# Optimization experiments

Measured on AMD Instinct MI355X. Metric: run time of the kernel, lower is better.

Reference implementation:

```python
import jax, jax.numpy as jnp
from jax import lax
import numpy as np

RADIUS = 1
DILATION = 2
NUM_BINS = 16  # DualSimilarityLoss uses num_bins=16
ALPHA = 5.0
BETA = 0.1
NOISE = 1e-4


def _avg_pool2(x):
    b, c, h, w = x.shape
    return x.reshape(b, c, h // 2, 2, w // 2, 2).mean(axis=(3, 5))


def _conv_rep(x, k, pad):
    # replicate-pad then VALID conv, NCHW / OIHW
    xp = jnp.pad(x, ((0, 0), (0, 0), (pad, pad), (pad, pad)), mode='edge')
    return lax.conv_general_dilated(xp, k, (1, 1), 'VALID',
                                    dimension_numbers=('NCHW', 'OIHW', 'NCHW'))


def _upsample_align_corners(x, H, W):
    # bilinear, align_corners=True (matches F.interpolate(..., align_corners=True))
    b, c, h, w = x.shape

    def coords(n_out, n_in):
        pos = jnp.arange(n_out, dtype=x.dtype) * ((n_in - 1) / (n_out - 1))
        i0 = jnp.clip(jnp.floor(pos).astype(jnp.int32), 0, n_in - 2)
        return i0, pos - i0.astype(x.dtype)

    y0, fy = coords(H, h)
    x0, fx = coords(W, w)
    rows = x[:, :, y0, :] * (1.0 - fy)[None, None, :, None] \
         + x[:, :, y0 + 1, :] * fy[None, None, :, None]
    out = rows[:, :, :, x0] * (1.0 - fx) + rows[:, :, :, x0 + 1] * fx
    return out


def _compute_mind(img, key):
    B, _, H, W = img.shape
    img = _avg_pool2(img)                      # (B,1,H/2,W/2)
    img = img + NOISE * jax.random.normal(key, img.shape, img.dtype)
    h, w = img.shape[2], img.shape[3]
    pad = RADIUS * DILATION                    # 2
    k = 2 * RADIUS + 1                         # 3
    ones_k = jnp.ones((1, 1, k, k), img.dtype)
    padded = jnp.pad(img, ((0, 0), (0, 0), (pad, pad), (pad, pad)), mode='edge')
    patch_mean = lax.conv_general_dilated(padded, ones_k, (1, 1), 'VALID',
                                          dimension_numbers=('NCHW', 'OIHW', 'NCHW')) / (k * k)
    patch_mean = jnp.pad(patch_mean, ((0, 0), (0, 0), (pad, pad), (pad, pad)), mode='edge')
    c = pad
    center = padded[:, :, c:c + h, c:c + w]
    variance = (center - patch_mean[:, :, c:c + h, c:c + w]) ** 2
    variance = _conv_rep(variance, ones_k, RADIUS) / (k * k)
    variance = jnp.maximum(variance, 1e-4)
    descs = []
    for i in range(-RADIUS, RADIUS + 1):
        for j in range(-RADIUS, RADIUS + 1):
            if i == 0 and j == 0:
                continue
            dx, dy = i * DILATION, j * DILATION
            off = padded[:, :, c + dy:c + dy + h, c + dx:c + dx + w]
            diff = jnp.clip((center - off) ** 2 / (variance * 2 + 1e-6), 0.0, 50.0)
            descs.append(diff)
    m = jnp.exp(-jnp.concatenate(descs, axis=1))          # (B,8,h,w)
    m = m / (m.sum(axis=1, keepdims=True) + 1e-8)
    m = jnp.where(jnp.isnan(m), 0.0, m)
    if (h, w) != (H, W):
        m = _upsample_align_corners(m, H, W)
    return m


def _nmi_loss(x, y, kx, ky):
    B = x.shape[0]
    x = x[:, :, ::2, ::2]
    y = y[:, :, ::2, ::2]
    x = x + NOISE * jax.random.normal(kx, x.shape, x.dtype)
    y = y + NOISE * jax.random.normal(ky, y.shape, y.dtype)
    xf = jnp.clip((x.reshape(B, -1) + 1.0) / 2.0, 0.001, 0.999)
    yf = jnp.clip((y.reshape(B, -1) + 1.0) / 2.0, 0.001, 0.999)
    grid = jnp.linspace(0.0, 1.0, NUM_BINS + 1)
    xb = jnp.clip(jnp.searchsorted(grid, xf, side='left') - 1, 0, NUM_BINS - 1)
    yb = jnp.clip(jnp.searchsorted(grid, yf, side='left') - 1, 0, NUM_BINS - 1)
    idx = xb * NUM_BINS + yb                               # (B,N)
    hist = jnp.zeros((B, NUM_BINS * NUM_BINS), jnp.float32)
    hist = hist.at[jnp.arange(B)[:, None], idx].add(1.0)
    hist = hist.reshape(B, NUM_BINS, NUM_BINS)
    hist = hist / (hist.sum(axis=(1, 2), keepdims=True) + 1e-10)
    xh = hist.sum(axis=2)
    yh = hist.sum(axis=1)
    eps = 1e-5
    hist = hist + eps
    xh = xh + eps
    yh = yh + eps
    mi = jnp.sum(hist * (jnp.log(hist) - jnp.log(xh[:, :, None] * yh[:, None, :])), axis=(1, 2))
    hx = -jnp.sum(xh * jnp.log(xh), axis=1)
    hy = -jnp.sum(yh * jnp.log(yh), axis=1)
    se = hx + hy
    nmi = jnp.where(se < 1e-10, 0.0, 2.0 * mi / se)
    nmi = jnp.clip(nmi, -1.0, 1.0)
    return -jnp.clip(nmi.mean(), -1.0, 1.0)


def _reg_loss(flow, ku, kv):
    sx = jnp.array([[-1, 0, 1], [-2, 0, 2], [-1, 0, 1]], jnp.float32).reshape(1, 1, 3, 3)
    sy = jnp.array([[-1, -2, -1], [0, 0, 0], [1, 2, 1]], jnp.float32).reshape(1, 1, 3, 3)
    lp = jnp.array([[0, 1, 0], [1, -4, 1], [0, 1, 0]], jnp.float32).reshape(1, 1, 3, 3)
    f = _avg_pool2(flow)
    u = f[:, 0:1] + NOISE * jax.random.normal(ku, f[:, 0:1].shape, f.dtype)
    v = f[:, 1:2] + NOISE * jax.random.normal(kv, f[:, 1:2].shape, f.dtype)
    grad_mag = _conv_rep(u, sx, 1) ** 2 + _conv_rep(u, sy, 1) ** 2 \
             + _conv_rep(v, sx, 1) ** 2 + _conv_rep(v, sy, 1) ** 2
    lap_mag = _conv_rep(u, lp, 1) ** 2 + _conv_rep(v, lp, 1) ** 2
    return jnp.clip(grad_mag, 0.0, 100.0).mean() + jnp.clip(lap_mag, 0.0, 100.0).mean()


def _total_loss(fixed, moved, flow):
    fixed = jnp.where(jnp.isnan(fixed), 0.0, fixed)
    moved = jnp.where(jnp.isnan(moved), 0.0, moved)
    flow = jnp.where(jnp.isnan(flow), 0.0, flow)
    ks = jax.random.split(jax.random.key(42), 6)
    mi = _nmi_loss(fixed, moved, ks[0], ks[1])
    mx = _compute_mind(fixed, ks[2])
    my = _compute_mind(moved, ks[3])
    d = jnp.abs(mx - my)
    mind = jnp.where(jnp.isnan(d), 0.0, d).mean()
    reg = _reg_loss(flow, ks[4], ks[5])
    return mi + ALPHA * mind + BETA * reg


def setup_inputs() -> dict:
    key = jax.random.key(0)
    k1, k2, k3 = jax.random.split(key, 3)
    B, H, W = 8, 512, 512
    return {
        'fixed': jax.random.normal(k1, (B, 1, H, W), jnp.float32),
        'moved': jax.random.normal(k2, (B, 1, H, W), jnp.float32),
        'flow': jax.random.normal(k3, (B, 2, H, W), jnp.float32),
    }


def reference(fixed, moved, flow):
    return _total_loss(fixed, moved, flow)
```

## Files before the change

### kernel.cpp

```cpp
#include <hip/hip_runtime.h>
#include <cmath>

#define BATCH 8
#define HF 512
#define WF 512
#define HS 256
#define WS 256
#define PLANE_S (HS * WS)
#define PLANE_F (HF * WF)

#define NMIND_BLOCKS 2048
#define NREG_BLOCKS  512

#define OFF_HISTP 0
#define OFF_PMIND (2048 * 1024)
#define OFF_PGRAD (OFF_PMIND + NMIND_BLOCKS * 8)
#define OFF_PLAP  (OFF_PGRAD + NREG_BLOCKS * 8)
#define OFF_NMI   (OFF_PLAP + NREG_BLOCKS * 8)

#define IMG_R 23
#define IMG_S 24
#define T_R 20
#define T_S 21
#define V_R 18
#define V_S 19

#define RP 34
#define RS 35

__device__ __forceinline__ int clampi(int v, int lo, int hi) {
    return v < lo ? lo : (v > hi ? hi : v);
}

__device__ __forceinline__ int bin_of(float x) {
    float v = (x + 1.0f) * 0.5f;
    v = fminf(fmaxf(v, 0.001f), 0.999f);
    float t = v * 16.0f;
    float ft = floorf(t);
    int c = (int)ft + ((t > ft) ? 1 : 0);
    int b = c - 1;
    return b < 0 ? 0 : (b > 15 ? 15 : b);
}

__global__ __launch_bounds__(256, 4) void fused_main_kernel(
    const float* __restrict__ fixed, const float* __restrict__ moved,
    const float* __restrict__ flow,
    unsigned* __restrict__ hist_part, double* __restrict__ pmind,
    double* __restrict__ pgrad, double* __restrict__ plap)
{
    __shared__ float S[4524];
    __shared__ unsigned lh[256];
    __shared__ float red[256];
    int tid = threadIdx.x;

    if (blockIdx.z < 2) {
        int idx = blockIdx.z * 256 + blockIdx.y * 16 + blockIdx.x;
        int b = idx >> 6, t64 = idx & 63;
        int y0p = (t64 >> 3) * 32, x0p = (t64 & 7) * 32;
        float* U = S;
        float* V = S + RP * RS;
        const float* ur = flow + (size_t)(b * 2) * PLANE_F;
        const float* vr = ur + PLANE_F;
        for (int i = tid; i < RP * RP; i += 256) {
            int r = i / RP, c = i - r * RP;
            int gy = clampi(y0p - 1 + r, 0, HS - 1);
            int gx = clampi(x0p - 1 + c, 0, WS - 1);
            const float* uu = ur + (size_t)(gy * 2) * WF + (size_t)(gx * 2);
            const float* vv = vr + (size_t)(gy * 2) * WF + (size_t)(gx * 2);
            float2 u0 = *(const float2*)uu, u1 = *(const float2*)(uu + WF);
            float2 v0 = *(const float2*)vv, v1 = *(const float2*)(vv + WF);
            U[r * RS + c] = (u0.x + u0.y + u1.x + u1.y) * 0.25f;
            V[r * RS + c] = (v0.x + v0.y + v1.x + v1.y) * 0.25f;
        }
        __syncthreads();
        float g = 0.f, l = 0.f;
        for (int k = tid; k < 32 * 32; k += 256) {
            int y = k >> 5, x = k & 31;
            const float* u0 = &U[y * RS + x];
            const float* v0 = &V[y * RS + x];
            float a00 = u0[0],      a01 = u0[1],          a02 = u0[2];
            float a10 = u0[RS],     a11 = u0[RS + 1],     a12 = u0[RS + 2];
            float a20 = u0[2 * RS], a21 = u0[2 * RS + 1], a22 = u0[2 * RS + 2];
            float c00 = v0[0],      c01 = v0[1],          c02 = v0[2];
            float c10 = v0[RS],     c11 = v0[RS + 1],     c12 = v0[RS + 2];
            float c20 = v0[2 * RS], c21 = v0[2 * RS + 1], c22 = v0[2 * RS + 2];
            float gxu = (a02 - a00) + 2.f * (a12 - a10) + (a22 - a20);
            float gyu = (a20 - a00) + 2.f * (a21 - a01) + (a22 - a02);
            float gxv = (c02 - c00) + 2.f * (c12 - c10) + (c22 - c20);
            float gyv = (c20 - c00) + 2.f * (c21 - c01) + (c22 - c02);
            float lpu = a01 + a10 - 4.f * a11 + a12 + a21;
            float lpv = c01 + c10 - 4.f * c11 + c12 + c21;
            float grad = gxu * gxu + gyu * gyu + gxv * gxv + gyv * gyv;
            float lap = lpu * lpu + lpv * lpv;
            g += fminf(grad, 100.f);
            l += fminf(lap, 100.f);
        }
        red[tid] = g;
        __syncthreads();
        for (int s = 128; s > 0; s >>= 1) { if (tid < s) red[tid] += red[tid + s]; __syncthreads(); }
        if (tid == 0) pgrad[b * 64 + t64] = (double)red[0];
        __syncthreads();
        red[tid] = l;
        __syncthreads();
        for (int s = 128; s > 0; s >>= 1) { if (tid < s) red[tid] += red[tid + s]; __syncthreads(); }
        if (tid == 0) plap[b * 64 + t64] = (double)red[0];
        return;
    }

    const float FS = (float)(255.0 / 511.0);
    int tx = blockIdx.x, ty = blockIdx.y, b = blockIdx.z - 2;
    int Xb = tx * 32, Yb = ty * 32;
    int dbx = (int)((float)Xb * FS);
    int dby = (int)((float)Yb * FS);
    int ibx = dbx - 3, iby = dby - 3;

    float* imgF = S;
    float* imgM = S + IMG_R * IMG_S;
    float* varF = S + 2 * IMG_R * IMG_S;
    float* varM = varF + V_R * V_S;
    float* diff = varM + V_R * V_S;
    float* tF   = diff;
    float* tM   = diff + T_R * T_S;

    lh[tid] = 0u;
    __syncthreads();

    const float* fb = fixed + (size_t)b * PLANE_F;
    const float* mb = moved + (size_t)b * PLANE_F;
    int oy0 = ty * 16, ox0 = tx * 16;
    for (int i = tid; i < IMG_R * IMG_R; i += 256) {
        int r = i / IMG_R, c = i - r * IMG_R;
        int gy = iby + r, gx = ibx + c;
        int cy = clampi(gy, 0, HS - 1), cx = clampi(gx, 0, WS - 1);
        const float* fp = fb + (size_t)(cy * 2) * WF + (size_t)(cx * 2);
        const float* mp = mb + (size_t)(cy * 2) * WF + (size_t)(cx * 2);
        float2 f0 = *(const float2*)fp;
        float2 f1 = *(const float2*)(fp + WF);
        float2 m0 = *(const float2*)mp;
        float2 m1 = *(const float2*)(mp + WF);
        imgF[r * IMG_S + c] = (f0.x + f0.y + f1.x + f1.y) * 0.25f;
        imgM[r * IMG_S + c] = (m0.x + m0.y + m1.x + m1.y) * 0.25f;
        if ((unsigned)(gy - oy0) < 16u && (unsigned)(gx - ox0) < 16u) {
            atomicAdd(&lh[bin_of(f0.x) * 16 + bin_of(m0.x)], 1u);
        }
    }
    __syncthreads();
    hist_part[((size_t)(b * 256 + ty * 16 + tx)) * 256 + tid] = lh[tid];

    const float NINTH = 1.0f / 9.0f;
    for (int i = tid; i < T_R * T_R; i += 256) {
        int r = i / T_R, c = i - r * T_R;
        float sF = 0.f, sM = 0.f;
        #pragma unroll
        for (int dy = 0; dy < 3; dy++)
            #pragma unroll
            for (int dx = 0; dx < 3; dx++) {
                sF += imgF[(r + dy) * IMG_S + c + dx];
                sM += imgM[(r + dy) * IMG_S + c + dx];
            }
        float dF = imgF[(r + 2) * IMG_S + c + 2] - sF * NINTH;
        float dM = imgM[(r + 2) * IMG_S + c + 2] - sM * NINTH;
        tF[r * T_S + c] = dF * dF;
        tM[r * T_S + c] = dM * dM;
    }
    __syncthreads();

    for (int i = tid; i < V_R * V_R; i += 256) {
        int r = i / V_R, c = i - r * V_R;
        float sF = 0.f, sM = 0.f;
        #pragma unroll
        for (int dy = 0; dy < 3; dy++)
            #pragma unroll
            for (int dx = 0; dx < 3; dx++) {
                sF += tF[(r + dy) * T_S + c + dx];
                sM += tM[(r + dy) * T_S + c + dx];
            }
        varF[r * V_S + c] = fmaxf(sF * NINTH, 1e-4f);
        varM[r * V_S + c] = fmaxf(sM * NINTH, 1e-4f);
    }
    __syncthreads();

    for (int i = tid; i < V_R * V_R; i += 256) {
        int r = i / V_R, c = i - r * V_R;
        float cF = imgF[(r + 3) * IMG_S + c + 3];
        float cM = imgM[(r + 3) * IMG_S + c + 3];
        float dF2 = 2.f * varF[r * V_S + c] + 1e-6f;
        float dM2 = 2.f * varM[r * V_S + c] + 1e-6f;
        float invF = 1.0f / dF2;
        float invM = 1.0f / dM2;
        float eF[8], eM[8];
        float sF = 0.f, sM = 0.f;
        int ch = 0;
        #pragma unroll
        for (int ii = -1; ii <= 1; ii++) {
            #pragma unroll
            for (int jj = -1; jj <= 1; jj++) {
                if (ii == 0 && jj == 0) continue;
                float aF = cF - imgF[(r + 3 + 2 * jj) * IMG_S + (c + 3 + 2 * ii)];
                float aM = cM - imgM[(r + 3 + 2 * jj) * IMG_S + (c + 3 + 2 * ii)];
                float qF = fminf(aF * aF * invF, 50.f);
                float qM = fminf(aM * aM * invM, 50.f);
                float vF_ = expf(-qF), vM_ = expf(-qM);
                eF[ch] = vF_; eM[ch] = vM_;
                sF += vF_; sM += vM_;
                ch++;
            }
        }
        float wF = 1.f / (sF + 1e-8f);
        float wM = 1.f / (sM + 1e-8f);
        float* dp = diff + (size_t)(r * V_S + c) * 8;
        #pragma unroll
        for (int q = 0; q < 8; q++) dp[q] = eF[q] * wF - eM[q] * wM;
    }
    __syncthreads();

    float local = 0.f;
    for (int k = tid; k < 32 * 32; k += 256) {
        int dy = k >> 5, dx = k & 31;
        float py = (float)(Yb + dy) * FS;
        int y0 = (int)py; if (y0 > HS - 2) y0 = HS - 2;
        float fy = py - (float)y0;
        float px = (float)(Xb + dx) * FS;
        int x0 = (int)px; if (x0 > WS - 2) x0 = WS - 2;
        float fx = px - (float)x0;
        const float* p00 = diff + (size_t)((y0 - dby) * V_S + (x0 - dbx)) * 8;
        const float* p10 = p00 + V_S * 8;
        #pragma unroll
        for (int q = 0; q < 8; q++) {
            float a  = p00[q]     * (1.f - fy) + p10[q]     * fy;
            float c2 = p00[q + 8] * (1.f - fy) + p10[q + 8] * fy;
            local += fabsf(a * (1.f - fx) + c2 * fx);
        }
    }
    red[tid] = local;
    __syncthreads();
    for (int s = 128; s > 0; s >>= 1) { if (tid < s) red[tid] += red[tid + s]; __syncthreads(); }
    if (tid == 0) pmind[b * 256 + ty * 16 + tx] = (double)red[0];
}

__global__ void nmi_kernel(const unsigned* __restrict__ hist_part, float* __restrict__ nmi_out) {
    int b = blockIdx.x;
    int t = threadIdx.x;
    __shared__ float p[256];
    __shared__ float xh[16], yh[16];
    __shared__ float red[256];
    unsigned hv = 0;
    const unsigned* hp = hist_part + (size_t)b * 256 * 256 + t;
    for (int i = 0; i < 256; i++) hv += hp[i * 256];
    float pv = (float)hv / 65536.0f;
    p[t] = pv;
    __syncthreads();
    if (t < 16) {
        float s = 0.f;
        for (int j = 0; j < 16; j++) s += p[t * 16 + j];
        xh[t] = s;
    } else if (t < 32) {
        int j = t - 16;
        float s = 0.f;
        for (int i = 0; i < 16; i++) s += p[i * 16 + j];
        yh[j] = s;
    }
    __syncthreads();
    const float eps = 1e-5f;
    int i = t >> 4, j = t & 15;
    float h = pv + eps;
    float mi_term = h * (logf(h) - logf((xh[i] + eps) * (yh[j] + eps)));
    red[t] = mi_term;
    __syncthreads();
    for (int s = 128; s > 0; s >>= 1) { if (t < s) red[t] += red[t + s]; __syncthreads(); }
    float mi = red[0];
    __syncthreads();
    float e_term = 0.f;
    if (t < 16) { float xe = xh[t] + eps; e_term = -xe * logf(xe); }
    else if (t < 32) { float ye = yh[t - 16] + eps; e_term = -ye * logf(ye); }
    red[t] = e_term;
    __syncthreads();
    for (int s = 128; s > 0; s >>= 1) { if (t < s) red[t] += red[t + s]; __syncthreads(); }
    if (t == 0) {
        float se = red[0];
        float nmi = (se < 1e-10f) ? 0.f : 2.f * mi / se;
        nmi_out[b] = fminf(fmaxf(nmi, -1.f), 1.f);
    }
}

__global__ void final_kernel(const float* __restrict__ nmi, const double* __restrict__ pmind,
                             const double* __restrict__ pgrad, const double* __restrict__ plap,
                             float* __restrict__ out) {
    __shared__ double red[256];
    int t = threadIdx.x;
    double sm = 0.0;
    for (int i = t; i < NMIND_BLOCKS; i += 256) sm += pmind[i];
    double sg = 0.0, sl = 0.0;
    for (int i = t; i < NREG_BLOCKS; i += 256) { sg += pgrad[i]; sl += plap[i]; }
    red[t] = sm;
    __syncthreads();
    for (int s = 128; s > 0; s >>= 1) { if (t < s) red[t] += red[t + s]; __syncthreads(); }
    double mind_sum = red[0];
    __syncthreads();
    red[t] = sg;
    __syncthreads();
    for (int s = 128; s > 0; s >>= 1) { if (t < s) red[t] += red[t + s]; __syncthreads(); }
    double grad_sum = red[0];
    __syncthreads();
    red[t] = sl;
    __syncthreads();
    for (int s = 128; s > 0; s >>= 1) { if (t < s) red[t] += red[t + s]; __syncthreads(); }
    double lap_sum = red[0];
    if (t == 0) {
        float s = 0.f;
        for (int b = 0; b < BATCH; b++) s += nmi[b];
        s /= (float)BATCH;
        s = fminf(fmaxf(s, -1.f), 1.f);
        double mi_loss = -(double)s;
        double mind_mean = mind_sum / (64.0 * (double)PLANE_F);
        double reg = grad_sum / (double)(BATCH * PLANE_S) + lap_sum / (double)(BATCH * PLANE_S);
        out[0] = (float)(mi_loss + 5.0 * mind_mean + 0.1 * reg);
    }
}

extern "C" void kernel_launch(void* const* d_in, const int* in_sizes, int n_in,
                              void* d_out, int out_size, void* d_ws, size_t ws_size,
                              hipStream_t stream) {
    const float* fixed = (const float*)d_in[0];
    const float* moved = (const float*)d_in[1];
    const float* flow  = (const float*)d_in[2];
    float* out = (float*)d_out;
    char* ws = (char*)d_ws;

    unsigned* hist_part = (unsigned*)(ws + OFF_HISTP);
    double*   pmind     = (double*)(ws + OFF_PMIND);
    double*   pgrad     = (double*)(ws + OFF_PGRAD);
    double*   plap      = (double*)(ws + OFF_PLAP);
    float*    nmi       = (float*)(ws + OFF_NMI);

    fused_main_kernel<<<dim3(16, 16, 10), 256, 0, stream>>>(fixed, moved, flow,
                                                            hist_part, pmind, pgrad, plap);
    nmi_kernel<<<BATCH, 256, 0, stream>>>(hist_part, nmi);
    final_kernel<<<1, 256, 0, stream>>>(nmi, pmind, pgrad, plap, out);
}
```

Baseline: 112.5 us.

## Accumulate joint histogram with global atomics and merge NMI into final kernel

Each block now adds its local histogram into a per-batch global histogram with atomics instead of writing a 2 MB partial histogram array. This removes the per-batch reduction over 256 partials. The separate NMI and final kernels are merged into one single-block tail kernel, and a small zero-init kernel is added. The cost is atomic contention on 8x256 counters and an extra tiny launch, in exchange for less global traffic and one fewer reduction kernel.

Result: slower. 121.7 us (+8.2%).

```diff
diff --git a/kernel.cpp b/kernel.cpp
--- a/kernel.cpp
+++ b/kernel.cpp
@@ -12,11 +12,10 @@
 #define NMIND_BLOCKS 2048
 #define NREG_BLOCKS  512
 
-#define OFF_HISTP 0
-#define OFF_PMIND (2048 * 1024)
+#define OFF_HIST  0
+#define OFF_PMIND 8192
 #define OFF_PGRAD (OFF_PMIND + NMIND_BLOCKS * 8)
 #define OFF_PLAP  (OFF_PGRAD + NREG_BLOCKS * 8)
-#define OFF_NMI   (OFF_PLAP + NREG_BLOCKS * 8)
 
 #define IMG_R 23
 #define IMG_S 24
@@ -42,10 +41,14 @@
     return b < 0 ? 0 : (b > 15 ? 15 : b);
 }
 
+__global__ void init_hist_kernel(unsigned* __restrict__ hist) {
+    hist[blockIdx.x * 256 + threadIdx.x] = 0u;
+}
+
 __global__ __launch_bounds__(256, 4) void fused_main_kernel(
     const float* __restrict__ fixed, const float* __restrict__ moved,
     const float* __restrict__ flow,
-    unsigned* __restrict__ hist_part, double* __restrict__ pmind,
+    unsigned* __restrict__ hist, double* __restrict__ pmind,
     double* __restrict__ pgrad, double* __restrict__ plap)
 {
     __shared__ float S[4524];
@@ -145,7 +148,7 @@
         }
     }
     __syncthreads();
-    hist_part[((size_t)(b * 256 + ty * 16 + tx)) * 256 + tid] = lh[tid];
+    if (lh[tid]) atomicAdd(&hist[b * 256 + tid], lh[tid]);
 
     const float NINTH = 1.0f / 9.0f;
     for (int i = tid; i < T_R * T_R; i += 256) {
@@ -238,56 +241,54 @@
     if (tid == 0) pmind[b * 256 + ty * 16 + tx] = (double)red[0];
 }
 
-__global__ void nmi_kernel(const unsigned* __restrict__ hist_part, float* __restrict__ nmi_out) {
-    int b = blockIdx.x;
+__global__ void tail_kernel(const unsigned* __restrict__ hist,
+                            const double* __restrict__ pmind,
+                            const double* __restrict__ pgrad, const double* __restrict__ plap,
+                            float* __restrict__ out) {
     int t = threadIdx.x;
     __shared__ float p[256];
     __shared__ float xh[16], yh[16];
-    __shared__ float red[256];
-    unsigned hv = 0;
-    const unsigned* hp = hist_part + (size_t)b * 256 * 256 + t;
-    for (int i = 0; i < 256; i++) hv += hp[i * 256];
-    float pv = (float)hv / 65536.0f;
-    p[t] = pv;
-    __syncthreads();
-    if (t < 16) {
-        float s = 0.f;
-        for (int j = 0; j < 16; j++) s += p[t * 16 + j];
-        xh[t] = s;
-    } else if (t < 32) {
-        int j = t - 16;
-        float s = 0.f;
-        for (int i = 0; i < 16; i++) s += p[i * 16 + j];
-        yh[j] = s;
-    }
-    __syncthreads();
+    __shared__ float redf[256];
+    __shared__ double red[256];
+
+    float nmi_sum = 0.f;
     const float eps = 1e-5f;
-    int i = t >> 4, j = t & 15;
-    float h = pv + eps;
-    float mi_term = h * (logf(h) - logf((xh[i] + eps) * (yh[j] + eps)));
-    red[t] = mi_term;
-    __syncthreads();
-    for (int s = 128; s > 0; s >>= 1) { if (t < s) red[t] += red[t + s]; __syncthreads(); }
-    float mi = red[0];
-    __syncthreads();
-    float e_term = 0.f;
-    if (t < 16) { float xe = xh[t] + eps; e_term = -xe * logf(xe); }
-    else if (t < 32) { float ye = yh[t - 16] + eps; e_term = -ye * logf(ye); }
-    red[t] = e_term;
-    __syncthreads();
-    for (int s = 128; s > 0; s >>= 1) { if (t < s) red[t] += red[t + s]; __syncthreads(); }
-    if (t == 0) {
-        float se = red[0];
+    for (int b = 0; b < BATCH; b++) {
+        unsigned hv = hist[b * 256 + t];
+        float pv = (float)hv / 65536.0f;
+        p[t] = pv;
+        __syncthreads();
+        if (t < 16) {
+            float s = 0.f;
+            for (int j = 0; j < 16; j++) s += p[t * 16 + j];
+            xh[t] = s;
+        } else if (t < 32) {
+            int j = t - 16;
+            float s = 0.f;
+            for (int i = 0; i < 16; i++) s += p[i * 16 + j];
+            yh[j] = s;
+        }
+        __syncthreads();
+        int i = t >> 4, j = t & 15;
+        float h = pv + eps;
+        float mi_term = h * (logf(h) - logf((xh[i] + eps) * (yh[j] + eps)));
+        redf[t] = mi_term;
+        __syncthreads();
+        for (int s = 128; s > 0; s >>= 1) { if (t < s) redf[t] += redf[t + s]; __syncthreads(); }
+        float mi = redf[0];
+        __syncthreads();
+        float e_term = 0.f;
+        if (t < 16) { float xe = xh[t] + eps; e_term = -xe * logf(xe); }
+        else if (t < 32) { float ye = yh[t - 16] + eps; e_term = -ye * logf(ye); }
+        redf[t] = e_term;
+        __syncthreads();
+        for (int s = 128; s > 0; s >>= 1) { if (t < s) redf[t] += redf[t + s]; __syncthreads(); }
+        float se = redf[0];
         float nmi = (se < 1e-10f) ? 0.f : 2.f * mi / se;
-        nmi_out[b] = fminf(fmaxf(nmi, -1.f), 1.f);
-    }
-}
-
-__global__ void final_kernel(const float* __restrict__ nmi, const double* __restrict__ pmind,
-                             const double* __restrict__ pgrad, const double* __restrict__ plap,
-                             float* __restrict__ out) {
-    __shared__ double red[256];
-    int t = threadIdx.x;
+        nmi_sum += fminf(fmaxf(nmi, -1.f), 1.f);
+        __syncthreads();
+    }
+
     double sm = 0.0;
     for (int i = t; i < NMIND_BLOCKS; i += 256) sm += pmind[i];
     double sg = 0.0, sl = 0.0;
@@ -307,9 +308,7 @@
     for (int s = 128; s > 0; s >>= 1) { if (t < s) red[t] += red[t + s]; __syncthreads(); }
     double lap_sum = red[0];
     if (t == 0) {
-        float s = 0.f;
-        for (int b = 0; b < BATCH; b++) s += nmi[b];
-        s /= (float)BATCH;
+        float s = nmi_sum / (float)BATCH;
         s = fminf(fmaxf(s, -1.f), 1.f);
         double mi_loss = -(double)s;
         double mind_mean = mind_sum / (64.0 * (double)PLANE_F);
@@ -327,14 +326,13 @@
     float* out = (float*)d_out;
     char* ws = (char*)d_ws;
 
-    unsigned* hist_part = (unsigned*)(ws + OFF_HISTP);
-    double*   pmind     = (double*)(ws + OFF_PMIND);
-    double*   pgrad     = (double*)(ws + OFF_PGRAD);
-    double*   plap      = (double*)(ws + OFF_PLAP);
-    float*    nmi       = (float*)(ws + OFF_NMI);
-
+    unsigned* hist  = (unsigned*)(ws + OFF_HIST);
+    double*   pmind = (double*)(ws + OFF_PMIND);
+    double*   pgrad = (double*)(ws + OFF_PGRAD);
+    double*   plap  = (double*)(ws + OFF_PLAP);
+
+    init_hist_kernel<<<dim3(8), 256, 0, stream>>>(hist);
     fused_main_kernel<<<dim3(16, 16, 10), 256, 0, stream>>>(fixed, moved, flow,
-                                                            hist_part, pmind, pgrad, plap);
-    nmi_kernel<<<BATCH, 256, 0, stream>>>(hist_part, nmi);
-    final_kernel<<<1, 256, 0, stream>>>(nmi, pmind, pgrad, plap, out);
-}
+                                                            hist, pmind, pgrad, plap);
+    tail_kernel<<<1, 256, 0, stream>>>(hist, pmind, pgrad, plap, out);
+}
```
